# Optimization experiments

Hardware: AMD Instinct MI355X
Metric: run time of the kernel (lower is better)

Reference implementation:

```python
import jax, jax.numpy as jnp
import numpy as np

# Equal-sized graph batches (batch vectors are sorted, contiguous segments)
B, NX, NY = 16, 1024, 4096   # clouds, coarse pts/cloud, fine pts/cloud
C, CS, H = 256, 128, 256     # coarse feat dim, skip feat dim, MLP hidden
EPS = 1e-8


def setup_inputs() -> dict:
    key = jax.random.key(0)
    ks = jax.random.split(key, 8)
    x = jax.random.normal(ks[0], (B * NX, C), dtype=jnp.float32)
    pos = jax.random.normal(ks[1], (B * NX, 3), dtype=jnp.float32)
    x_skip = jax.random.normal(ks[2], (B * NY, CS), dtype=jnp.float32)
    pos_skip = jax.random.normal(ks[3], (B * NY, 3), dtype=jnp.float32)
    batch = jnp.repeat(jnp.arange(B, dtype=jnp.int32), NX)
    batch_skip = jnp.repeat(jnp.arange(B, dtype=jnp.int32), NY)
    W1 = jax.random.normal(ks[4], (C + CS, H), dtype=jnp.float32) * 0.05
    b1 = jnp.zeros((H,), dtype=jnp.float32)
    W2 = jax.random.normal(ks[5], (H, H), dtype=jnp.float32) * 0.05
    b2 = jnp.zeros((H,), dtype=jnp.float32)
    return {"x": x, "pos": pos, "batch": batch, "x_skip": x_skip,
            "pos_skip": pos_skip, "batch_skip": batch_skip,
            "W1": W1, "b1": b1, "W2": W2, "b2": b2, "k": 3}


def knn_interpolate(x, pos, pos_skip, k):
    # Reshape flat batched point sets into [B, n, .] (batch vectors are
    # contiguous equal-sized segments, so this matches the per-batch loop).
    fx = x.reshape(B, NX, C)
    px = pos.reshape(B, NX, 3)
    py = pos_skip.reshape(B, NY, 3)
    # Squared distances via the Gram trick: [B, NY, NX]
    d2 = (jnp.sum(py * py, -1)[:, :, None]
          + jnp.sum(px * px, -1)[:, None, :]
          - 2.0 * jnp.einsum('byd,bxd->byx', py, px))
    neg_d2, idx = jax.lax.top_k(-d2, k)            # k nearest (smallest d2)
    dist = jnp.sqrt(jnp.maximum(-neg_d2, 0.0))     # [B, NY, k]
    w = 1.0 / (dist + EPS)
    gathered = jax.vmap(lambda f, i: f[i])(fx, idx)  # [B, NY, k, C]
    num = jnp.einsum('byk,bykc->byc', w, gathered)
    den = jnp.sum(w, axis=-1, keepdims=True) + EPS
    return (num / den).reshape(B * NY, C)


def reference(x, pos, batch, x_skip, pos_skip, batch_skip, W1, b1, W2, b2, k):
    interp = knn_interpolate(x, pos, pos_skip, k)      # [B*NY, C]
    h = jnp.concatenate([interp, x_skip], axis=1)      # [B*NY, C+CS]
    h = jax.nn.relu(h @ W1 + b1)
    h = jax.nn.relu(h @ W2 + b2)
    return h
```

## Files before the change

### kernel.cpp

```cpp
#include <hip/hip_runtime.h>
#include <hip/hip_bf16.h>

#define B_  16
#define NX_ 1024
#define NY_ 4096
#define C_  256
#define CS_ 128
#define H_  256
#define M_  (B_ * NY_)
#define K1_ (C_ + CS_)
#define K2_ (H_)

using short8  = __attribute__((ext_vector_type(8))) short;
using floatx4 = __attribute__((ext_vector_type(4))) float;

__device__ __forceinline__ unsigned short f2bf(float f) {
    unsigned int u = __float_as_uint(f);
    unsigned int r = (u + 0x7fffu + ((u >> 16) & 1u)) >> 16;
    return (unsigned short)r;
}

__global__ __launch_bounds__(256) void knn_interp_kernel(
    const float* __restrict__ x, const float* __restrict__ pos,
    const float* __restrict__ x_skip, const float* __restrict__ pos_skip,
    unsigned short* __restrict__ h0)
{
    __shared__ float spx[NX_], spy[NX_], spz[NX_], spn[NX_];
    const int tid  = threadIdx.x;
    const int wave = tid >> 6;
    const int lane = tid & 63;
    const int b    = blockIdx.x >> 10;

    for (int j = tid; j < NX_; j += 256) {
        const float* pp = pos + (size_t)(b * NX_ + j) * 3;
        float px = pp[0], py = pp[1], pz = pp[2];
        spx[j] = px; spy[j] = py; spz[j] = pz;
        spn[j] = __fadd_rn(__fadd_rn(__fmul_rn(px, px), __fmul_rn(py, py)),
                           __fmul_rn(pz, pz));
    }
    __syncthreads();

    const int y = blockIdx.x * 4 + wave;
    const float* q = pos_skip + (size_t)y * 3;
    const float qx = q[0], qy = q[1], qz = q[2];
    const float qn = __fadd_rn(__fadd_rn(__fmul_rn(qx, qx), __fmul_rn(qy, qy)),
                               __fmul_rn(qz, qz));

    float bd0 = 3.4e38f, bd1 = 3.4e38f, bd2 = 3.4e38f;
    int   bi0 = 0x7fffffff, bi1 = 0x7fffffff, bi2 = 0x7fffffff;
    #pragma unroll
    for (int t = 0; t < NX_ / 64; ++t) {
        const int j = lane + t * 64;
        float dot = __fadd_rn(__fadd_rn(__fmul_rn(qx, spx[j]),
                                        __fmul_rn(qy, spy[j])),
                              __fmul_rn(qz, spz[j]));
        float d2 = __fsub_rn(__fadd_rn(qn, spn[j]), __fmul_rn(2.0f, dot));
        if (d2 < bd2) {
            if (d2 < bd1) {
                bd2 = bd1; bi2 = bi1;
                if (d2 < bd0) { bd1 = bd0; bi1 = bi0; bd0 = d2; bi0 = j; }
                else          { bd1 = d2;  bi1 = j; }
            } else { bd2 = d2; bi2 = j; }
        }
    }

    float nd0, nd1, nd2; int ni0, ni1, ni2;
    #pragma unroll
    for (int kk = 0; kk < 3; ++kk) {
        float cd = bd0; int ci = bi0;
        #pragma unroll
        for (int m = 1; m < 64; m <<= 1) {
            float od = __shfl_xor(cd, m);
            int   oi = __shfl_xor(ci, m);
            if (od < cd || (od == cd && oi < ci)) { cd = od; ci = oi; }
        }
        if (kk == 0) { nd0 = cd; ni0 = ci; }
        else if (kk == 1) { nd1 = cd; ni1 = ci; }
        else { nd2 = cd; ni2 = ci; }
        if (bi0 == ci) {
            bd0 = bd1; bi0 = bi1;
            bd1 = bd2; bi1 = bi2;
            bd2 = 3.4e38f; bi2 = 0x7fffffff;
        }
    }

    const float w0 = 1.0f / (sqrtf(fmaxf(nd0, 0.0f)) + 1e-8f);
    const float w1 = 1.0f / (sqrtf(fmaxf(nd1, 0.0f)) + 1e-8f);
    const float w2 = 1.0f / (sqrtf(fmaxf(nd2, 0.0f)) + 1e-8f);
    const float inv_den = 1.0f / (w0 + w1 + w2 + 1e-8f);

    const float* fb = x + (size_t)b * NX_ * C_;
    const float4 f0 = *(const float4*)(fb + (size_t)ni0 * C_ + lane * 4);
    const float4 f1 = *(const float4*)(fb + (size_t)ni1 * C_ + lane * 4);
    const float4 f2 = *(const float4*)(fb + (size_t)ni2 * C_ + lane * 4);

    ushort4 o;
    o.x = f2bf((w0 * f0.x + w1 * f1.x + w2 * f2.x) * inv_den);
    o.y = f2bf((w0 * f0.y + w1 * f1.y + w2 * f2.y) * inv_den);
    o.z = f2bf((w0 * f0.z + w1 * f1.z + w2 * f2.z) * inv_den);
    o.w = f2bf((w0 * f0.w + w1 * f1.w + w2 * f2.w) * inv_den);
    *(ushort4*)(h0 + (size_t)y * K1_ + lane * 4) = o;

    const float2 s2 = *(const float2*)(x_skip + (size_t)y * CS_ + lane * 2);
    ushort2 os;
    os.x = f2bf(s2.x);
    os.y = f2bf(s2.y);
    *(ushort2*)(h0 + (size_t)y * K1_ + C_ + lane * 2) = os;
}

__global__ __launch_bounds__(256) void prep_w(
    const float* __restrict__ W1, const float* __restrict__ W2,
    unsigned short* __restrict__ W1t, unsigned short* __restrict__ W2t)
{
    int id = blockIdx.x * 256 + threadIdx.x;
    if (id < K1_ * H_) {
        int n = id / K1_, k = id - n * K1_;
        W1t[id] = f2bf(W1[(size_t)k * H_ + n]);
    }
    if (id < K2_ * H_) {
        int n = id >> 8, k = id & 255;
        W2t[id] = f2bf(W2[(size_t)k * H_ + n]);
    }
}

template<int K, int OUT_BF16>
__global__ __launch_bounds__(256) void gemm_bias_relu(
    const unsigned short* __restrict__ A,
    const unsigned short* __restrict__ Bt,
    const float* __restrict__ bias,
    void* __restrict__ outp)
{
    constexpr int LDSK = 48;
    __shared__ unsigned short As[64 * LDSK];
    __shared__ unsigned short Bs[64 * LDSK];

    const int tid  = threadIdx.x;
    const int lane = tid & 63;
    const int wave = tid >> 6;
    const int wr = wave >> 1, wc = wave & 1;
    const int m0 = blockIdx.x * 64;
    const int n0 = blockIdx.y * 64;

    const int lrow = tid >> 2;
    const int lcol = (tid & 3) * 8;
    const unsigned short* Ag = A  + (size_t)(m0 + lrow) * K + lcol;
    const unsigned short* Bg = Bt + (size_t)(n0 + lrow) * K + lcol;
    unsigned short* AsW = As + lrow * LDSK + lcol;
    unsigned short* BsW = Bs + lrow * LDSK + lcol;

    const int r16 = lane & 15, qk = lane >> 4;
    const unsigned short* AsR = As + (wr * 32 + r16) * LDSK + qk * 8;
    const unsigned short* BsR = Bs + (wc * 32 + r16) * LDSK + qk * 8;

    floatx4 acc[2][2] = {};

    for (int kt = 0; kt < K; kt += 32) {
        const uint4 av = *(const uint4*)(Ag + kt);
        const uint4 bv = *(const uint4*)(Bg + kt);
        __syncthreads();
        *(uint4*)AsW = av;
        *(uint4*)BsW = bv;
        __syncthreads();
        short8 a0 = *(const short8*)(AsR);
        short8 a1 = *(const short8*)(AsR + 16 * LDSK);
        short8 b0 = *(const short8*)(BsR);
        short8 b1 = *(const short8*)(BsR + 16 * LDSK);
        acc[0][0] = __builtin_amdgcn_mfma_f32_16x16x32_bf16(a0, b0, acc[0][0], 0, 0, 0);
        acc[0][1] = __builtin_amdgcn_mfma_f32_16x16x32_bf16(a0, b1, acc[0][1], 0, 0, 0);
        acc[1][0] = __builtin_amdgcn_mfma_f32_16x16x32_bf16(a1, b0, acc[1][0], 0, 0, 0);
        acc[1][1] = __builtin_amdgcn_mfma_f32_16x16x32_bf16(a1, b1, acc[1][1], 0, 0, 0);
    }

    #pragma unroll
    for (int m = 0; m < 2; ++m) {
        #pragma unroll
        for (int n = 0; n < 2; ++n) {
            const int gc = n0 + wc * 32 + n * 16 + r16;
            const float bv = bias[gc];
            #pragma unroll
            for (int r = 0; r < 4; ++r) {
                const int gr = m0 + wr * 32 + m * 16 + qk * 4 + r;
                float v = acc[m][n][r] + bv;
                v = fmaxf(v, 0.0f);
                if (OUT_BF16)
                    ((unsigned short*)outp)[(size_t)gr * H_ + gc] = f2bf(v);
                else
                    ((float*)outp)[(size_t)gr * H_ + gc] = v;
            }
        }
    }
}

extern "C" void kernel_launch(void* const* d_in, const int* in_sizes, int n_in,
                              void* d_out, int out_size, void* d_ws, size_t ws_size,
                              hipStream_t stream)
{
    const float* x        = (const float*)d_in[0];
    const float* pos      = (const float*)d_in[1];
    const float* x_skip   = (const float*)d_in[3];
    const float* pos_skip = (const float*)d_in[4];
    const float* W1       = (const float*)d_in[6];
    const float* b1       = (const float*)d_in[7];
    const float* W2       = (const float*)d_in[8];
    const float* b2       = (const float*)d_in[9];

    char* ws = (char*)d_ws;
    unsigned short* h0  = (unsigned short*)(ws);
    unsigned short* h1  = (unsigned short*)(ws + 50331648);
    unsigned short* W1t = (unsigned short*)(ws + 50331648 + 33554432);
    unsigned short* W2t = (unsigned short*)(ws + 83886080 + 196608);

    hipLaunchKernelGGL(knn_interp_kernel, dim3(M_ / 4), dim3(256), 0, stream,
                       x, pos, x_skip, pos_skip, h0);
    hipLaunchKernelGGL(prep_w, dim3((K1_ * H_ + 255) / 256), dim3(256), 0, stream,
                       W1, W2, W1t, W2t);
    hipLaunchKernelGGL((gemm_bias_relu<K1_, 1>), dim3(M_ / 64, H_ / 64), dim3(256),
                       0, stream, h0, W1t, b1, h1);
    hipLaunchKernelGGL((gemm_bias_relu<K2_, 0>), dim3(M_ / 64, H_ / 64), dim3(256),
                       0, stream, h1, W2t, b2, (float*)d_out);
}
```

Baseline: 234.1 us.

## Split kNN into per-thread select and gather, retile GEMM with async LDS double buffering

kNN search now assigns one query per thread, with two halves scanning 512 points each and merging their top-3 lists through shared memory. This replaces the wave-per-query scan and its shuffle reductions. A separate gather kernel builds the bf16 concat row from the stored indices and weights. The GEMM now has each block compute a 64x256 tile with 16 MFMA accumulators per wave, loading tiles with global_load_lds into double-buffered, XOR-swizzled shared memory. This removes the redundant A loads across column blocks but raises register and LDS usage, and adds an extra kernel plus a round trip of intermediate data through memory.

```diff
diff --git a/kernel.cpp b/kernel.cpp
--- a/kernel.cpp
+++ b/kernel.cpp
@@ -20,27 +20,35 @@
     return (unsigned short)r;
 }
 
-__global__ __launch_bounds__(256) void knn_interp_kernel(
-    const float* __restrict__ x, const float* __restrict__ pos,
-    const float* __restrict__ x_skip, const float* __restrict__ pos_skip,
-    unsigned short* __restrict__ h0)
-{
-    __shared__ float spx[NX_], spy[NX_], spz[NX_], spn[NX_];
+typedef const __attribute__((address_space(1))) void gas_t;
+typedef __attribute__((address_space(3))) void las_t;
+__device__ __forceinline__ void gload_lds16(const void* g, void* l) {
+    __builtin_amdgcn_global_load_lds((gas_t*)g, (las_t*)l, 16, 0, 0);
+}
+
+__global__ __launch_bounds__(512) void knn_select(
+    const float* __restrict__ pos, const float* __restrict__ pos_skip,
+    int4* __restrict__ idx4, float4* __restrict__ wgt4)
+{
+    __shared__ float4 sp[NX_];
+    __shared__ float  m_d[3][256];
+    __shared__ int    m_i[3][256];
+
     const int tid  = threadIdx.x;
-    const int wave = tid >> 6;
-    const int lane = tid & 63;
-    const int b    = blockIdx.x >> 10;
-
-    for (int j = tid; j < NX_; j += 256) {
+    const int p    = tid & 255;
+    const int half = tid >> 8;
+    const int y    = blockIdx.x * 256 + p;
+    const int b    = y >> 12;
+
+    for (int j = tid; j < NX_; j += 512) {
         const float* pp = pos + (size_t)(b * NX_ + j) * 3;
         float px = pp[0], py = pp[1], pz = pp[2];
-        spx[j] = px; spy[j] = py; spz[j] = pz;
-        spn[j] = __fadd_rn(__fadd_rn(__fmul_rn(px, px), __fmul_rn(py, py)),
-                           __fmul_rn(pz, pz));
+        float pn = __fadd_rn(__fadd_rn(__fmul_rn(px, px), __fmul_rn(py, py)),
+                             __fmul_rn(pz, pz));
+        sp[j] = make_float4(px, py, pz, pn);
     }
     __syncthreads();
 
-    const int y = blockIdx.x * 4 + wave;
     const float* q = pos_skip + (size_t)y * 3;
     const float qx = q[0], qy = q[1], qz = q[2];
     const float qn = __fadd_rn(__fadd_rn(__fmul_rn(qx, qx), __fmul_rn(qy, qy)),
@@ -48,13 +56,15 @@
 
     float bd0 = 3.4e38f, bd1 = 3.4e38f, bd2 = 3.4e38f;
     int   bi0 = 0x7fffffff, bi1 = 0x7fffffff, bi2 = 0x7fffffff;
-    #pragma unroll
-    for (int t = 0; t < NX_ / 64; ++t) {
-        const int j = lane + t * 64;
-        float dot = __fadd_rn(__fadd_rn(__fmul_rn(qx, spx[j]),
-                                        __fmul_rn(qy, spy[j])),
-                              __fmul_rn(qz, spz[j]));
-        float d2 = __fsub_rn(__fadd_rn(qn, spn[j]), __fmul_rn(2.0f, dot));
+    const int j0 = half * 512;
+    #pragma unroll 4
+    for (int t = 0; t < 512; ++t) {
+        const int j = j0 + t;
+        const float4 pv = sp[j];
+        float dot = __fadd_rn(__fadd_rn(__fmul_rn(qx, pv.x),
+                                        __fmul_rn(qy, pv.y)),
+                              __fmul_rn(qz, pv.z));
+        float d2 = __fsub_rn(__fadd_rn(qn, pv.w), __fmul_rn(2.0f, dot));
         if (d2 < bd2) {
             if (d2 < bd1) {
                 bd2 = bd1; bi2 = bi1;
@@ -64,47 +74,63 @@
         }
     }
 
-    float nd0, nd1, nd2; int ni0, ni1, ni2;
-    #pragma unroll
-    for (int kk = 0; kk < 3; ++kk) {
-        float cd = bd0; int ci = bi0;
-        #pragma unroll
-        for (int m = 1; m < 64; m <<= 1) {
-            float od = __shfl_xor(cd, m);
-            int   oi = __shfl_xor(ci, m);
-            if (od < cd || (od == cd && oi < ci)) { cd = od; ci = oi; }
-        }
-        if (kk == 0) { nd0 = cd; ni0 = ci; }
-        else if (kk == 1) { nd1 = cd; ni1 = ci; }
-        else { nd2 = cd; ni2 = ci; }
-        if (bi0 == ci) {
-            bd0 = bd1; bi0 = bi1;
-            bd1 = bd2; bi1 = bi2;
-            bd2 = 3.4e38f; bi2 = 0x7fffffff;
-        }
-    }
-
-    const float w0 = 1.0f / (sqrtf(fmaxf(nd0, 0.0f)) + 1e-8f);
-    const float w1 = 1.0f / (sqrtf(fmaxf(nd1, 0.0f)) + 1e-8f);
-    const float w2 = 1.0f / (sqrtf(fmaxf(nd2, 0.0f)) + 1e-8f);
-    const float inv_den = 1.0f / (w0 + w1 + w2 + 1e-8f);
-
-    const float* fb = x + (size_t)b * NX_ * C_;
-    const float4 f0 = *(const float4*)(fb + (size_t)ni0 * C_ + lane * 4);
-    const float4 f1 = *(const float4*)(fb + (size_t)ni1 * C_ + lane * 4);
-    const float4 f2 = *(const float4*)(fb + (size_t)ni2 * C_ + lane * 4);
+    if (half == 1) {
+        m_d[0][p] = bd0; m_d[1][p] = bd1; m_d[2][p] = bd2;
+        m_i[0][p] = bi0; m_i[1][p] = bi1; m_i[2][p] = bi2;
+    }
+    __syncthreads();
+    if (half == 0) {
+        const float a0 = bd0, a1 = bd1, a2 = bd2;
+        const int   ia0 = bi0, ia1 = bi1, ia2 = bi2;
+        const float b0 = m_d[0][p], b1 = m_d[1][p], b2 = m_d[2][p];
+        const int   ib0 = m_i[0][p], ib1 = m_i[1][p], ib2 = m_i[2][p];
+        float d0, d1, d2; int n0, n1, n2;
+        if (a0 <= b0) {
+            d0 = a0; n0 = ia0;
+            if (a1 <= b0) { d1 = a1; n1 = ia1;
+                bool c = (a2 <= b0); d2 = c ? a2 : b0; n2 = c ? ia2 : ib0; }
+            else          { d1 = b0; n1 = ib0;
+                bool c = (a1 <= b1); d2 = c ? a1 : b1; n2 = c ? ia1 : ib1; }
+        } else {
+            d0 = b0; n0 = ib0;
+            if (a0 <= b1) { d1 = a0; n1 = ia0;
+                bool c = (a1 <= b1); d2 = c ? a1 : b1; n2 = c ? ia1 : ib1; }
+            else          { d1 = b1; n1 = ib1;
+                bool c = (a0 <= b2); d2 = c ? a0 : b2; n2 = c ? ia0 : ib2; }
+        }
+        const float w0 = 1.0f / (sqrtf(fmaxf(d0, 0.0f)) + 1e-8f);
+        const float w1 = 1.0f / (sqrtf(fmaxf(d1, 0.0f)) + 1e-8f);
+        const float w2 = 1.0f / (sqrtf(fmaxf(d2, 0.0f)) + 1e-8f);
+        const float inv_den = 1.0f / (w0 + w1 + w2 + 1e-8f);
+        idx4[y] = make_int4(n0, n1, n2, 0);
+        wgt4[y] = make_float4(w0, w1, w2, inv_den);
+    }
+}
+
+__global__ __launch_bounds__(256) void gather_concat(
+    const float* __restrict__ x, const float* __restrict__ x_skip,
+    const int4* __restrict__ idx4, const float4* __restrict__ wgt4,
+    unsigned short* __restrict__ h0)
+{
+    const int wave = threadIdx.x >> 6, lane = threadIdx.x & 63;
+    const int y = blockIdx.x * 4 + wave;
+    const int4  id = idx4[y];
+    const float4 w = wgt4[y];
+    const float* fb = x + (size_t)(y >> 12) * (NX_ * C_);
+
+    const float4 f0 = *(const float4*)(fb + (size_t)id.x * C_ + lane * 4);
+    const float4 f1 = *(const float4*)(fb + (size_t)id.y * C_ + lane * 4);
+    const float4 f2 = *(const float4*)(fb + (size_t)id.z * C_ + lane * 4);
 
     ushort4 o;
-    o.x = f2bf((w0 * f0.x + w1 * f1.x + w2 * f2.x) * inv_den);
-    o.y = f2bf((w0 * f0.y + w1 * f1.y + w2 * f2.y) * inv_den);
-    o.z = f2bf((w0 * f0.z + w1 * f1.z + w2 * f2.z) * inv_den);
-    o.w = f2bf((w0 * f0.w + w1 * f1.w + w2 * f2.w) * inv_den);
+    o.x = f2bf((w.x * f0.x + w.y * f1.x + w.z * f2.x) * w.w);
+    o.y = f2bf((w.x * f0.y + w.y * f1.y + w.z * f2.y) * w.w);
+    o.z = f2bf((w.x * f0.z + w.y * f1.z + w.z * f2.z) * w.w);
+    o.w = f2bf((w.x * f0.w + w.y * f1.w + w.z * f2.w) * w.w);
     *(ushort4*)(h0 + (size_t)y * K1_ + lane * 4) = o;
 
     const float2 s2 = *(const float2*)(x_skip + (size_t)y * CS_ + lane * 2);
-    ushort2 os;
-    os.x = f2bf(s2.x);
-    os.y = f2bf(s2.y);
+    ushort2 os; os.x = f2bf(s2.x); os.y = f2bf(s2.y);
     *(ushort2*)(h0 + (size_t)y * K1_ + C_ + lane * 2) = os;
 }
 
@@ -130,58 +156,82 @@
     const float* __restrict__ bias,
     void* __restrict__ outp)
 {
-    constexpr int LDSK = 48;
-    __shared__ unsigned short As[64 * LDSK];
-    __shared__ unsigned short Bs[64 * LDSK];
+    __shared__ unsigned short As[2][64 * 64];
+    __shared__ unsigned short Bs[2][256 * 64];
 
     const int tid  = threadIdx.x;
     const int lane = tid & 63;
     const int wave = tid >> 6;
-    const int wr = wave >> 1, wc = wave & 1;
-    const int m0 = blockIdx.x * 64;
-    const int n0 = blockIdx.y * 64;
-
-    const int lrow = tid >> 2;
-    const int lcol = (tid & 3) * 8;
-    const unsigned short* Ag = A  + (size_t)(m0 + lrow) * K + lcol;
-    const unsigned short* Bg = Bt + (size_t)(n0 + lrow) * K + lcol;
-    unsigned short* AsW = As + lrow * LDSK + lcol;
-    unsigned short* BsW = Bs + lrow * LDSK + lcol;
-
-    const int r16 = lane & 15, qk = lane >> 4;
-    const unsigned short* AsR = As + (wr * 32 + r16) * LDSK + qk * 8;
-    const unsigned short* BsR = Bs + (wc * 32 + r16) * LDSK + qk * 8;
-
-    floatx4 acc[2][2] = {};
-
-    for (int kt = 0; kt < K; kt += 32) {
-        const uint4 av = *(const uint4*)(Ag + kt);
-        const uint4 bv = *(const uint4*)(Bg + kt);
+    const int m0   = blockIdx.x * 64;
+    const int r16  = lane & 15, qk = lane >> 4;
+
+    floatx4 acc[4][4] = {};
+
+    auto stage = [&](int buf, int kt) {
+        #pragma unroll
+        for (int i = 0; i < 2; ++i) {
+            const int row  = (tid >> 3) + i * 32;
+            const int slot = (tid & 7) ^ (row & 7);
+            gload_lds16(A + (size_t)(m0 + row) * K + kt + slot * 8,
+                        &As[buf][row * 64 + (tid & 7) * 8]);
+        }
+        #pragma unroll
+        for (int i = 0; i < 8; ++i) {
+            const int row  = (tid >> 3) + i * 32;
+            const int slot = (tid & 7) ^ (row & 7);
+            gload_lds16(Bt + (size_t)row * K + kt + slot * 8,
+                        &Bs[buf][row * 64 + (tid & 7) * 8]);
+        }
+    };
+
+    auto compute = [&](int buf) {
+        #pragma unroll
+        for (int s = 0; s < 2; ++s) {
+            short8 af[4], bf[4];
+            #pragma unroll
+            for (int m = 0; m < 4; ++m) {
+                const int row  = m * 16 + r16;
+                const int slot = (s * 4 + qk) ^ (r16 & 7);
+                af[m] = *(const short8*)&As[buf][row * 64 + slot * 8];
+            }
+            #pragma unroll
+            for (int n = 0; n < 4; ++n) {
+                const int row  = wave * 64 + n * 16 + r16;
+                const int slot = (s * 4 + qk) ^ (r16 & 7);
+                bf[n] = *(const short8*)&Bs[buf][row * 64 + slot * 8];
+            }
+            #pragma unroll
+            for (int m = 0; m < 4; ++m)
+                #pragma unroll
+                for (int n = 0; n < 4; ++n)
+                    acc[m][n] = __builtin_amdgcn_mfma_f32_16x16x32_bf16(
+                        af[m], bf[n], acc[m][n], 0, 0, 0);
+        }
+    };
+
+    stage(0, 0);
+    __syncthreads();
+    int cur = 0;
+    constexpr int NT = K / 64;
+    #pragma unroll
+    for (int t = 1; t < NT; ++t) {
+        stage(cur ^ 1, t * 64);
+        compute(cur);
         __syncthreads();
-        *(uint4*)AsW = av;
-        *(uint4*)BsW = bv;
-        __syncthreads();
-        short8 a0 = *(const short8*)(AsR);
-        short8 a1 = *(const short8*)(AsR + 16 * LDSK);
-        short8 b0 = *(const short8*)(BsR);
-        short8 b1 = *(const short8*)(BsR + 16 * LDSK);
-        acc[0][0] = __builtin_amdgcn_mfma_f32_16x16x32_bf16(a0, b0, acc[0][0], 0, 0, 0);
-        acc[0][1] = __builtin_amdgcn_mfma_f32_16x16x32_bf16(a0, b1, acc[0][1], 0, 0, 0);
-        acc[1][0] = __builtin_amdgcn_mfma_f32_16x16x32_bf16(a1, b0, acc[1][0], 0, 0, 0);
-        acc[1][1] = __builtin_amdgcn_mfma_f32_16x16x32_bf16(a1, b1, acc[1][1], 0, 0, 0);
-    }
+        cur ^= 1;
+    }
+    compute(cur);
 
     #pragma unroll
-    for (int m = 0; m < 2; ++m) {
-        #pragma unroll
-        for (int n = 0; n < 2; ++n) {
-            const int gc = n0 + wc * 32 + n * 16 + r16;
-            const float bv = bias[gc];
+    for (int n = 0; n < 4; ++n) {
+        const int gc = wave * 64 + n * 16 + r16;
+        const float bv = bias[gc];
+        #pragma unroll
+        for (int m = 0; m < 4; ++m) {
             #pragma unroll
             for (int r = 0; r < 4; ++r) {
-                const int gr = m0 + wr * 32 + m * 16 + qk * 4 + r;
-                float v = acc[m][n][r] + bv;
-                v = fmaxf(v, 0.0f);
+                const int gr = m0 + m * 16 + qk * 4 + r;
+                float v = fmaxf(acc[m][n][r] + bv, 0.0f);
                 if (OUT_BF16)
                     ((unsigned short*)outp)[(size_t)gr * H_ + gc] = f2bf(v);
                 else
@@ -207,15 +257,19 @@
     char* ws = (char*)d_ws;
     unsigned short* h0  = (unsigned short*)(ws);
     unsigned short* h1  = (unsigned short*)(ws + 50331648);
-    unsigned short* W1t = (unsigned short*)(ws + 50331648 + 33554432);
-    unsigned short* W2t = (unsigned short*)(ws + 83886080 + 196608);
-
-    hipLaunchKernelGGL(knn_interp_kernel, dim3(M_ / 4), dim3(256), 0, stream,
-                       x, pos, x_skip, pos_skip, h0);
+    unsigned short* W1t = (unsigned short*)(ws + 83886080);
+    unsigned short* W2t = (unsigned short*)(ws + 84082688);
+    int4*           idx4 = (int4*)(ws + 84213760);
+    float4*         wgt4 = (float4*)(ws + 85262336);
+
+    hipLaunchKernelGGL(knn_select, dim3(M_ / 256), dim3(512), 0, stream,
+                       pos, pos_skip, idx4, wgt4);
+    hipLaunchKernelGGL(gather_concat, dim3(M_ / 4), dim3(256), 0, stream,
+                       x, x_skip, idx4, wgt4, h0);
     hipLaunchKernelGGL(prep_w, dim3((K1_ * H_ + 255) / 256), dim3(256), 0, stream,
                        W1, W2, W1t, W2t);
-    hipLaunchKernelGGL((gemm_bias_relu<K1_, 1>), dim3(M_ / 64, H_ / 64), dim3(256),
+    hipLaunchKernelGGL((gemm_bias_relu<K1_, 1>), dim3(M_ / 64), dim3(256),
                        0, stream, h0, W1t, b1, h1);
-    hipLaunchKernelGGL((gemm_bias_relu<K2_, 0>), dim3(M_ / 64, H_ / 64), dim3(256),
+    hipLaunchKernelGGL((gemm_bias_relu<K2_, 0>), dim3(M_ / 64), dim3(256),
                        0, stream, h1, W2t, b2, (float*)d_out);
 }
```

After: 230.2 us. About the same (-1.7%).
